# Kernel tuning notes

Hardware: AMD Instinct MI355X
Metric: run time of the kernel (lower is better)

Reference implementation:

```python
import jax, jax.numpy as jnp
import numpy as np

E, H, D = 512, 8, 64          # embed_dim, num_heads, head_dim
MAX_SUM = 128                  # max_summary (embedding table has MAX_SUM+1 rows, row 0 = padding)
SCALE = D ** -0.5


def _linear(x, w, b):
    y = jnp.einsum('...i,oi->...o', x, w)
    return y if b is None else y + b


def setup_inputs() -> dict:
    key = jax.random.key(0)
    ks = jax.random.split(key, 16)
    R, B, S = 2048, 2, 128

    def xav(k, shape, gain=1.0):
        fan_in, fan_out = shape[1], shape[0]
        a = gain * np.sqrt(6.0 / (fan_in + fan_out))
        return jax.random.uniform(k, shape, jnp.float32, -a, a)

    g = 1.0 / np.sqrt(2.0)
    embed_table = jax.random.normal(ks[0], (MAX_SUM + 1, E), jnp.float32) * 0.02
    embed_table = embed_table.at[0].set(0.0)  # padding_idx=0
    return {
        'reg_x': jax.random.normal(ks[1], (R, B, E), jnp.float32),
        'sum_token_ids': jax.random.randint(ks[2], (B, S), 0, MAX_SUM),
        'sum_len': S,
        'reg_len': R,
        'embed_table': embed_table,
        'wq1': xav(ks[3], (E, E), g), 'bq1': jnp.zeros((E,), jnp.float32),
        'wq2': xav(ks[4], (E, E), g), 'bq2': jnp.zeros((E,), jnp.float32),
        'wk': xav(ks[5], (E, E), g),  'bk': jnp.zeros((E,), jnp.float32),
        'wv': xav(ks[6], (E, E), g),  'bv': jnp.zeros((E,), jnp.float32),
        'wo': xav(ks[7], (E, E)),     'bo': jnp.zeros((E,), jnp.float32),
        'sum_gate_w': xav(ks[8], (E, E)),
        'reg_gate_w': xav(ks[9], (E, E)),
        'gate_bias': jax.random.normal(ks[10], (E,), jnp.float32),
    }


def reference(reg_x, sum_token_ids, sum_len, reg_len, embed_table,
              wq1, bq1, wq2, bq2, wk, bk, wv, bv, wo, bo,
              sum_gate_w, reg_gate_w, gate_bias):
    R, B, _ = reg_x.shape
    S = sum_token_ids.shape[1]

    # regular keys/values (shared across all stages)
    reg_k = _linear(reg_x, wk, bk).reshape(R, B, H, D)
    reg_v = _linear(reg_x, wv, bv).reshape(R, B, H, D)

    # ---- stage 1: summary queries (learned summary embeddings) attend to regular tokens
    sum_q = embed_table[sum_token_ids.T].reshape(S, B, H, D)  # [S,B,H,D]
    scores_sr = jnp.einsum('sbhd,rbhd->bhsr', sum_q * SCALE, reg_k)
    w_sr = jax.nn.softmax(scores_sr, axis=-1)
    sum_x2 = jnp.einsum('bhsr,rbhd->sbhd', w_sr, reg_v)       # summary K=V for stage 2

    # ---- stage 2: regular queries attend to summary tokens
    reg_q1 = _linear(reg_x, wq1, bq1).reshape(R, B, H, D)
    scores_rs = jnp.einsum('rbhd,sbhd->bhrs', reg_q1 * SCALE, sum_x2)
    w_rs = jax.nn.softmax(scores_rs, axis=-1)
    sum_output = jnp.einsum('bhrs,sbhd->rbhd', w_rs, sum_x2).reshape(R, B, E)

    # ---- stage 3: regular self-attention
    reg_q2 = _linear(reg_x, wq2, bq2).reshape(R, B, H, D)
    scores_rr = jnp.einsum('qbhd,kbhd->bhqk', reg_q2 * SCALE, reg_k)
    w_rr = jax.nn.softmax(scores_rr, axis=-1)
    reg_output = jnp.einsum('bhqk,kbhd->qbhd', w_rr, reg_v).reshape(R, B, E)

    # ---- gated fusion of summary path and regular path
    gate = jax.nn.sigmoid(_linear(sum_output, sum_gate_w, None)
                          + _linear(reg_output, reg_gate_w, None) + gate_bias)
    attn_output = gate * sum_output + (1.0 - gate) * reg_output
    return _linear(attn_output, wo, bo)
```

## Files before the change

### kernel.cpp

```cpp
#include <hip/hip_runtime.h>
#include <cstdint>
#include <cstddef>

constexpr int R_ = 2048;
constexpr int B_ = 2;
constexpr int S_ = 128;
constexpr int E_ = 512;
constexpr int H_ = 8;
constexpr int D_ = 64;
constexpr int N_ = R_ * B_;
constexpr float SCALE_ = 0.125f;
constexpr float LOG2E_ = 1.44269504088896340736f;
constexpr float SLOG2E_ = SCALE_ * LOG2E_;

typedef short bf8_t __attribute__((ext_vector_type(8)));
typedef float f32x4 __attribute__((ext_vector_type(4)));
typedef float f32x16 __attribute__((ext_vector_type(16)));
typedef unsigned u32x4 __attribute__((ext_vector_type(4)));

#define MFMA16(a, b, c) __builtin_amdgcn_mfma_f32_16x16x32_bf16((a), (b), (c), 0, 0, 0)
#define MFMA32(a, b, c) __builtin_amdgcn_mfma_f32_32x32x16_bf16((a), (b), (c), 0, 0, 0)

__device__ __forceinline__ unsigned short f2bf(float f) {
  unsigned u = __builtin_bit_cast(unsigned, f);
  unsigned r = u + 0x7FFFu + ((u >> 16) & 1u);
  return (unsigned short)(r >> 16);
}
__device__ __forceinline__ float bf2f(unsigned short h) {
  unsigned u = ((unsigned)h) << 16;
  return __builtin_bit_cast(float, u);
}
__device__ __forceinline__ int kvperm(int kv) {
  return (kv & ~15) | (kv & 3) | ((kv & 4) << 1) | ((kv & 8) >> 1);
}

struct WSplitJob { const float* src; unsigned short* dst; };
struct WSplit7 { WSplitJob j[7]; };

__global__ __launch_bounds__(256)
void fused_split_kernel(const float* __restrict__ reg_x, unsigned short* __restrict__ Apair,
                        WSplit7 P, const float* __restrict__ table,
                        const int* __restrict__ ids,
                        unsigned short* __restrict__ sqhi, unsigned short* __restrict__ sqlo)
{
  const int bx = blockIdx.x;
  const int tid = threadIdx.x;
  if (bx < 8192) {
    const int idx = bx * 256 + tid;
    const int r = idx >> 9, c = idx & 511;
    const float v = reg_x[idx];
    const unsigned short hi = f2bf(v);
    unsigned short* d = Apair + ((size_t)r << 10) + c;
    d[0] = hi; d[512] = f2bf(v - bf2f(hi));
  } else if (bx < 15360) {
    const int bj = bx - 8192;
    const WSplitJob jb = P.j[bj >> 10];
    const int idx = (bj & 1023) * 256 + tid;
    const int r = idx >> 9, c = idx & 511;
    const float v = jb.src[idx];
    const unsigned short hi = f2bf(v);
    const unsigned short lo = f2bf(v - bf2f(hi));
    unsigned short* d = jb.dst + (size_t)r * 1536 + c;
    d[0] = hi; d[512] = hi; d[1024] = lo;
  } else {
    const int idx = (bx - 15360) * 256 + tid;
    const int d = idx & 63;
    const int s = (idx >> 6) & 127;
    const int h = (idx >> 13) & 7;
    const int b = idx >> 16;
    const float v = table[(size_t)ids[b * S_ + s] * E_ + h * 64 + d] * SLOG2E_;
    const unsigned short hi = f2bf(v);
    sqhi[idx] = hi;
    sqlo[idx] = f2bf(v - bf2f(hi));
  }
}

struct GemmOut {
  const unsigned short* W;
  const float* bias;
  float scale;
  float* Cf;
  unsigned short* hi;
  unsigned short* lo;
  int mode;
};
struct GemmOuts4 { GemmOut o[4]; };

__global__ __launch_bounds__(256, 4)
void gemm_split_kernel(const unsigned short* __restrict__ A, GemmOuts4 P)
{
  const GemmOut g = P.o[blockIdx.z];
  __shared__ unsigned short As[128][48];
  __shared__ unsigned short Ws[64][48];

  const int tid = threadIdx.x;
  const int w = tid >> 6;
  const int l = tid & 63;
  const int lr = l & 15;
  const int lg = l >> 4;
  const int n0 = blockIdx.x * 128;
  const int o0 = blockIdx.y * 64;

  f32x4 acc[2][4];
#pragma unroll
  for (int m = 0; m < 2; ++m)
#pragma unroll
    for (int n = 0; n < 4; ++n) acc[m][n] = (f32x4){0.f, 0.f, 0.f, 0.f};

  const int ar = tid >> 1;
  const int ac = (tid & 1) * 16;
  const int wr = tid >> 2;
  const int wc = (tid & 3) * 8;

  bf8_t ra0 = *(const bf8_t*)(A + (size_t)(n0 + ar) * 1024 + ac);
  bf8_t ra1 = *(const bf8_t*)(A + (size_t)(n0 + ar) * 1024 + ac + 8);
  bf8_t rw0 = *(const bf8_t*)(g.W + (size_t)(o0 + wr) * 1536 + wc);

  for (int k0 = 0; k0 < 1536; k0 += 32) {
    __syncthreads();
    *(bf8_t*)&As[ar][ac] = ra0;
    *(bf8_t*)&As[ar][ac + 8] = ra1;
    *(bf8_t*)&Ws[wr][wc] = rw0;
    __syncthreads();
    if (k0 + 32 < 1536) {
      const int ak = (k0 + 32) & 1023;
      ra0 = *(const bf8_t*)(A + (size_t)(n0 + ar) * 1024 + ak + ac);
      ra1 = *(const bf8_t*)(A + (size_t)(n0 + ar) * 1024 + ak + ac + 8);
      rw0 = *(const bf8_t*)(g.W + (size_t)(o0 + wr) * 1536 + k0 + 32 + wc);
    }

    bf8_t bvs[4];
#pragma unroll
    for (int n = 0; n < 4; ++n)
      bvs[n] = *(const bf8_t*)&Ws[n * 16 + lr][lg * 8];
#pragma unroll
    for (int m = 0; m < 2; ++m) {
      bf8_t av = *(const bf8_t*)&As[w * 32 + m * 16 + lr][lg * 8];
#pragma unroll
      for (int n = 0; n < 4; ++n)
        acc[m][n] = MFMA16(av, bvs[n], acc[m][n]);
    }
  }

#pragma unroll
  for (int m = 0; m < 2; ++m)
#pragma unroll
    for (int n = 0; n < 4; ++n)
#pragma unroll
      for (int r = 0; r < 4; ++r) {
        const int row = n0 + w * 32 + m * 16 + lg * 4 + r;
        const int col = o0 + n * 16 + lr;
        float v = acc[m][n][r];
        if (g.bias) v += g.bias[col];
        v *= g.scale;
        if (g.mode == 0) {
          g.Cf[((size_t)row << 9) + col] = v;
        } else {
          const int bb = row & 1, rr = row >> 1;
          const int hh = col >> 6, dd = col & 63;
          size_t id;
          if (g.mode == 1) id = (((size_t)(bb * H_ + hh) * R_) + rr) * 64 + dd;
          else             id = (((size_t)(bb * H_ + hh) * 64) + dd) * R_ + kvperm(rr);
          const unsigned short hv = f2bf(v);
          g.hi[id] = hv;
          g.lo[id] = f2bf(v - bf2f(hv));
        }
      }
}

__global__ __launch_bounds__(256, 4)
void gate_blend_gemm_kernel(const unsigned short* __restrict__ A1,
                            const unsigned short* __restrict__ A2,
                            const unsigned short* __restrict__ W1,
                            const unsigned short* __restrict__ W2,
                            const float* __restrict__ gb,
                            unsigned short* __restrict__ attnP)
{
  __shared__ unsigned short As[128][48];
  __shared__ unsigned short Ws[64][48];

  const int tid = threadIdx.x;
  const int w = tid >> 6;
  const int l = tid & 63;
  const int lr = l & 15;
  const int lg = l >> 4;
  const int n0 = blockIdx.x * 128;
  const int o0 = blockIdx.y * 64;

  f32x4 acc[2][4];
#pragma unroll
  for (int m = 0; m < 2; ++m)
#pragma unroll
    for (int n = 0; n < 4; ++n) acc[m][n] = (f32x4){0.f, 0.f, 0.f, 0.f};

  const int ar = tid >> 1;
  const int ac = (tid & 1) * 16;
  const int wr = tid >> 2;
  const int wc = (tid & 3) * 8;

  auto aP = [&](int kk) {
    const unsigned short* Ax = (kk < 48) ? A1 : A2;
    const int k0 = ((kk < 48) ? kk : kk - 48) * 32;
    return Ax + (size_t)(n0 + ar) * 1024 + (k0 & 1023) + ac;
  };
  auto wP = [&](int kk) {
    const unsigned short* Wx = (kk < 48) ? W1 : W2;
    const int k0 = ((kk < 48) ? kk : kk - 48) * 32;
    return Wx + (size_t)(o0 + wr) * 1536 + k0 + wc;
  };

  bf8_t ra0 = *(const bf8_t*)aP(0);
  bf8_t ra1 = *(const bf8_t*)(aP(0) + 8);
  bf8_t rw0 = *(const bf8_t*)wP(0);

  for (int kk = 0; kk < 96; ++kk) {
    __syncthreads();
    *(bf8_t*)&As[ar][ac] = ra0;
    *(bf8_t*)&As[ar][ac + 8] = ra1;
    *(bf8_t*)&Ws[wr][wc] = rw0;
    __syncthreads();
    if (kk + 1 < 96) {
      ra0 = *(const bf8_t*)aP(kk + 1);
      ra1 = *(const bf8_t*)(aP(kk + 1) + 8);
      rw0 = *(const bf8_t*)wP(kk + 1);
    }

    bf8_t bvs[4];
#pragma unroll
    for (int n = 0; n < 4; ++n)
      bvs[n] = *(const bf8_t*)&Ws[n * 16 + lr][lg * 8];
#pragma unroll
    for (int m = 0; m < 2; ++m) {
      bf8_t av = *(const bf8_t*)&As[w * 32 + m * 16 + lr][lg * 8];
#pragma unroll
      for (int n = 0; n < 4; ++n)
        acc[m][n] = MFMA16(av, bvs[n], acc[m][n]);
    }
  }

#pragma unroll
  for (int m = 0; m < 2; ++m)
#pragma unroll
    for (int n = 0; n < 4; ++n)
#pragma unroll
      for (int r = 0; r < 4; ++r) {
        const int row = n0 + w * 32 + m * 16 + lg * 4 + r;
        const int col = o0 + n * 16 + lr;
        const float t = acc[m][n][r] + gb[col];
        const float gt = 1.0f / (1.0f + __expf(-t));
        const size_t base = (size_t)row << 10;
        const float so = bf2f(A1[base + col]) + bf2f(A1[base + 512 + col]);
        const float ro = bf2f(A2[base + col]) + bf2f(A2[base + 512 + col]);
        const float a = gt * so + (1.0f - gt) * ro;
        const unsigned short hv = f2bf(a);
        attnP[base + col] = hv;
        attnP[base + 512 + col] = f2bf(a - bf2f(hv));
      }
}

struct FArgs {
  const unsigned short *Qhi, *Qlo, *Khi, *Klo, *VtHi, *VtLo;
  int q_len, kv_len, chunk, zsplit, out_mode;
  float *accA, *accB, *mlP;
  unsigned short* OutP;
};

__device__ __forceinline__
void flash_body(const FArgs& A, const int bh, const int q0blk, const int c)
{
  __shared__ unsigned short KsH[64][72];
  __shared__ unsigned short KsL[64][72];
  __shared__ unsigned short VsH[64][72];
  __shared__ unsigned short VsL[64][72];

  const int tid = threadIdx.x;
  const int w = tid >> 6;
  const int l = tid & 63;
  const int lq = l & 31;
  const int hi = l >> 5;
  const int q0 = q0blk * 128;
  const int kvbeg = c * A.chunk;
  const int kvend = kvbeg + A.chunk;
  const int qrow = q0 + w * 32 + lq;

  bf8_t qh[4], ql[4];
  {
    const size_t qbase = ((size_t)bh * A.q_len + qrow) * 64;
#pragma unroll
    for (int kd = 0; kd < 4; ++kd) {
      qh[kd] = *(const bf8_t*)(A.Qhi + qbase + kd * 16 + hi * 8);
      ql[kd] = *(const bf8_t*)(A.Qlo + qbase + kd * 16 + hi * 8);
    }
  }

  f32x16 acc0 = {0,0,0,0,0,0,0,0,0,0,0,0,0,0,0,0};
  f32x16 acc1 = {0,0,0,0,0,0,0,0,0,0,0,0,0,0,0,0};
  float mrow = -INFINITY;
  float lrow = 0.0f;

  const int sr = tid >> 2;
  const int sc = (tid & 3) * 16;

  bf8_t rkh[2], rkl[2], rvh[2], rvl[2];
  {
    const size_t kb = ((size_t)bh * A.kv_len + kvbeg + sr) * 64 + sc;
    rkh[0] = *(const bf8_t*)(A.Khi + kb);  rkh[1] = *(const bf8_t*)(A.Khi + kb + 8);
    rkl[0] = *(const bf8_t*)(A.Klo + kb);  rkl[1] = *(const bf8_t*)(A.Klo + kb + 8);
    const size_t vb = ((size_t)bh * 64 + sr) * A.kv_len + kvbeg + sc;
    rvh[0] = *(const bf8_t*)(A.VtHi + vb); rvh[1] = *(const bf8_t*)(A.VtHi + vb + 8);
    rvl[0] = *(const bf8_t*)(A.VtLo + vb); rvl[1] = *(const bf8_t*)(A.VtLo + vb + 8);
  }

  for (int kv0 = kvbeg; kv0 < kvend; kv0 += 64) {
    __syncthreads();
    *(bf8_t*)&KsH[sr][sc] = rkh[0];  *(bf8_t*)&KsH[sr][sc + 8] = rkh[1];
    *(bf8_t*)&KsL[sr][sc] = rkl[0];  *(bf8_t*)&KsL[sr][sc + 8] = rkl[1];
    *(bf8_t*)&VsH[sr][sc] = rvh[0];  *(bf8_t*)&VsH[sr][sc + 8] = rvh[1];
    *(bf8_t*)&VsL[sr][sc] = rvl[0];  *(bf8_t*)&VsL[sr][sc + 8] = rvl[1];
    __syncthreads();
    if (kv0 + 64 < kvend) {
      const size_t kb = ((size_t)bh * A.kv_len + kv0 + 64 + sr) * 64 + sc;
      rkh[0] = *(const bf8_t*)(A.Khi + kb);  rkh[1] = *(const bf8_t*)(A.Khi + kb + 8);
      rkl[0] = *(const bf8_t*)(A.Klo + kb);  rkl[1] = *(const bf8_t*)(A.Klo + kb + 8);
      const size_t vb = ((size_t)bh * 64 + sr) * A.kv_len + kv0 + 64 + sc;
      rvh[0] = *(const bf8_t*)(A.VtHi + vb); rvh[1] = *(const bf8_t*)(A.VtHi + vb + 8);
      rvl[0] = *(const bf8_t*)(A.VtLo + vb); rvl[1] = *(const bf8_t*)(A.VtLo + vb + 8);
    }

    f32x16 s0 = {0,0,0,0,0,0,0,0,0,0,0,0,0,0,0,0};
    f32x16 s1 = {0,0,0,0,0,0,0,0,0,0,0,0,0,0,0,0};
    __builtin_amdgcn_s_setprio(1);
#pragma unroll
    for (int kd = 0; kd < 4; ++kd) {
      const bf8_t kfh0 = *(const bf8_t*)&KsH[lq][kd * 16 + hi * 8];
      const bf8_t kfl0 = *(const bf8_t*)&KsL[lq][kd * 16 + hi * 8];
      s0 = MFMA32(kfh0, qh[kd], s0);
      s0 = MFMA32(kfh0, ql[kd], s0);
      s0 = MFMA32(kfl0, qh[kd], s0);
      const bf8_t kfh1 = *(const bf8_t*)&KsH[32 + lq][kd * 16 + hi * 8];
      const bf8_t kfl1 = *(const bf8_t*)&KsL[32 + lq][kd * 16 + hi * 8];
      s1 = MFMA32(kfh1, qh[kd], s1);
      s1 = MFMA32(kfh1, ql[kd], s1);
      s1 = MFMA32(kfl1, qh[kd], s1);
    }
    __builtin_amdgcn_s_setprio(0);

    float mx = fmaxf(s0[0], s1[0]);
#pragma unroll
    for (int r = 1; r < 16; ++r) mx = fmaxf(mx, fmaxf(s0[r], s1[r]));
    mx = fmaxf(mx, __shfl_xor(mx, 32));
    if (mx > mrow + 8.0f) {
      const float f = exp2f(mrow - mx);
      mrow = mx;
      lrow *= f;
#pragma unroll
      for (int r = 0; r < 16; ++r) { acc0[r] *= f; acc1[r] *= f; }
    }
    float ts = 0.f;
#pragma unroll
    for (int r = 0; r < 16; ++r) { s0[r] = exp2f(s0[r] - mrow); ts += s0[r]; }
#pragma unroll
    for (int r = 0; r < 16; ++r) { s1[r] = exp2f(s1[r] - mrow); ts += s1[r]; }
    ts += __shfl_xor(ts, 32);
    lrow += ts;

    bf8_t pah[4], pal[4];
    const unsigned sel = 0x07060302u;
#pragma unroll
    for (int n = 0; n < 2; ++n)
#pragma unroll
      for (int ks = 0; ks < 2; ++ks) {
        u32x4 hp, lp;
#pragma unroll
        for (int p2 = 0; p2 < 4; ++p2) {
          const float a = n ? s1[ks * 8 + p2 * 2]     : s0[ks * 8 + p2 * 2];
          const float b = n ? s1[ks * 8 + p2 * 2 + 1] : s0[ks * 8 + p2 * 2 + 1];
          const unsigned ua = __builtin_bit_cast(unsigned, a);
          const unsigned ub = __builtin_bit_cast(unsigned, b);
          hp[p2] = __builtin_amdgcn_perm(ub, ua, sel);
          const float la = a - __builtin_bit_cast(float, ua & 0xFFFF0000u);
          const float lb = b - __builtin_bit_cast(float, ub & 0xFFFF0000u);
          lp[p2] = __builtin_amdgcn_perm(__builtin_bit_cast(unsigned, lb),
                                         __builtin_bit_cast(unsigned, la), sel);
        }
        pah[n * 2 + ks] = __builtin_bit_cast(bf8_t, hp);
        pal[n * 2 + ks] = __builtin_bit_cast(bf8_t, lp);
      }

    __builtin_amdgcn_s_setprio(1);
#pragma unroll
    for (int n = 0; n < 2; ++n)
#pragma unroll
      for (int ks = 0; ks < 2; ++ks) {
        const int vcol = n * 32 + ks * 16 + hi * 8;
        const bf8_t ph = pah[n * 2 + ks];
        const bf8_t pl = pal[n * 2 + ks];
        {
          const bf8_t vfh = *(const bf8_t*)&VsH[lq][vcol];
          const bf8_t vfl = *(const bf8_t*)&VsL[lq][vcol];
          acc0 = MFMA32(vfh, ph, acc0);
          acc0 = MFMA32(vfh, pl, acc0);
          acc0 = MFMA32(vfl, ph, acc0);
        }
        {
          const bf8_t vfh = *(const bf8_t*)&VsH[32 + lq][vcol];
          const bf8_t vfl = *(const bf8_t*)&VsL[32 + lq][vcol];
          acc1 = MFMA32(vfh, ph, acc1);
          acc1 = MFMA32(vfh, pl, acc1);
          acc1 = MFMA32(vfl, ph, acc1);
        }
      }
    __builtin_amdgcn_s_setprio(0);
  }

  if (A.out_mode == 0) {
    const size_t cstride = (size_t)16 * A.q_len * 64;
    float* accbase = (c < A.zsplit) ? A.accA + (size_t)c * cstride
                                    : A.accB + (size_t)(c - A.zsplit) * cstride;
    float* rowp = accbase + ((size_t)bh * A.q_len + qrow) * 64;
#pragma unroll
    for (int rg = 0; rg < 4; ++rg) {
      *(float4*)(rowp + rg * 8 + hi * 4) =
          make_float4(acc0[rg * 4 + 0], acc0[rg * 4 + 1], acc0[rg * 4 + 2], acc0[rg * 4 + 3]);
      *(float4*)(rowp + 32 + rg * 8 + hi * 4) =
          make_float4(acc1[rg * 4 + 0], acc1[rg * 4 + 1], acc1[rg * 4 + 2], acc1[rg * 4 + 3]);
    }
    if (l < 32) {
      const int q = q0 + w * 32 + l;
      *(float2*)&A.mlP[((size_t)(c * 16 + bh) * A.q_len + q) * 2] = make_float2(mrow, lrow);
    }
  } else {
    const float inv = 1.0f / lrow;
    const int b = bh >> 3, h = bh & 7;
    const size_t base = ((size_t)qrow * B_ + b) << 10;
#pragma unroll
    for (int hd = 0; hd < 2; ++hd)
#pragma unroll
      for (int rg = 0; rg < 4; ++rg) {
        const int col = h * 64 + hd * 32 + rg * 8 + hi * 4;
        ushort4 hv4, lv4;
#pragma unroll
        for (int i = 0; i < 4; ++i) {
          const float v = (hd ? acc1[rg * 4 + i] : acc0[rg * 4 + i]) * inv;
          const unsigned short hv = f2bf(v);
          ((unsigned short*)&hv4)[i] = hv;
          ((unsigned short*)&lv4)[i] = f2bf(v - bf2f(hv));
        }
        *(ushort4*)&A.OutP[base + col] = hv4;
        *(ushort4*)&A.OutP[base + 512 + col] = lv4;
      }
  }
}

__global__ __launch_bounds__(256, 2)
void flash_s1_kernel(FArgs a)
{
  flash_body(a, blockIdx.x, blockIdx.y, blockIdx.z);
}

__global__ __launch_bounds__(256, 2)
void flash_s23_kernel(FArgs a3, FArgs a2)
{
  const int bid = blockIdx.x;
  if (bid < 512) flash_body(a3, bid & 15, (bid >> 4) & 15, bid >> 8);
  else           flash_body(a2, bid & 15, ((bid - 512) >> 4) & 15, 0);
}

__global__ __launch_bounds__(256)
void merge_x2_kernel(const float* __restrict__ acc, const float* __restrict__ ml,
                     unsigned short* __restrict__ X2hi, unsigned short* __restrict__ X2lo,
                     unsigned short* __restrict__ X2Thi, unsigned short* __restrict__ X2Tlo)
{
  const int idx = blockIdx.x * 256 + threadIdx.x;
  const int d = idx & 63;
  const int q = (idx >> 6) & 127;
  const int bh = idx >> 13;
  float M = -INFINITY;
#pragma unroll
  for (int c = 0; c < 16; ++c)
    M = fmaxf(M, ml[((size_t)(c * 16 + bh) * 128 + q) * 2]);
  float ls = 0.f, o = 0.f;
#pragma unroll
  for (int c = 0; c < 16; ++c) {
    const size_t mi = ((size_t)(c * 16 + bh) * 128 + q) * 2;
    const float wgt = exp2f(ml[mi] - M);
    ls += wgt * ml[mi + 1];
    o += wgt * acc[(size_t)c * 131072 + ((size_t)bh * 128 + q) * 64 + d];
  }
  const float v = o / ls;
  const unsigned short hv = f2bf(v);
  const unsigned short lv = f2bf(v - bf2f(hv));
  X2hi[((size_t)bh * 128 + q) * 64 + d] = hv;
  X2lo[((size_t)bh * 128 + q) * 64 + d] = lv;
  const int qp = kvperm(q);
  X2Thi[((size_t)bh * 64 + d) * 128 + qp] = hv;
  X2Tlo[((size_t)bh * 64 + d) * 128 + qp] = lv;
}

__global__ __launch_bounds__(256)
void merge_rows_kernel(const float* __restrict__ accA, const float* __restrict__ accB,
                       const float* __restrict__ ml, unsigned short* __restrict__ OutP)
{
  const int idx = blockIdx.x * 256 + threadIdx.x;
  const int d = idx & 63;
  const int q = (idx >> 6) & 2047;
  const int bh = idx >> 17;
  const size_t mi0 = ((size_t)bh * 2048 + q) * 2;
  const size_t mi1 = ((size_t)(16 + bh) * 2048 + q) * 2;
  const float m0 = ml[mi0], m1 = ml[mi1];
  const float M = fmaxf(m0, m1);
  const float w0 = exp2f(m0 - M), w1 = exp2f(m1 - M);
  const float ls = w0 * ml[mi0 + 1] + w1 * ml[mi1 + 1];
  const size_t aoff = ((size_t)bh * 2048 + q) * 64 + d;
  const float v = (w0 * accA[aoff] + w1 * accB[aoff]) / ls;
  const int b = bh >> 3, h = bh & 7;
  const size_t nrow = (size_t)q * B_ + b;
  const int col = h * 64 + d;
  const unsigned short hv = f2bf(v);
  OutP[nrow * 1024 + col] = hv;
  OutP[nrow * 1024 + 512 + col] = f2bf(v - bf2f(hv));
}

extern "C" void kernel_launch(void* const* d_in, const int* in_sizes, int n_in,
                              void* d_out, int out_size, void* d_ws, size_t ws_size,
                              hipStream_t stream)
{
  const float* reg_x = (const float*)d_in[0];
  const int*   ids   = (const int*)d_in[1];
  const float* table = (const float*)d_in[4];
  const float* wq1 = (const float*)d_in[5];  const float* bq1 = (const float*)d_in[6];
  const float* wq2 = (const float*)d_in[7];  const float* bq2 = (const float*)d_in[8];
  const float* wk  = (const float*)d_in[9];  const float* bk  = (const float*)d_in[10];
  const float* wv  = (const float*)d_in[11]; const float* bv  = (const float*)d_in[12];
  const float* wo  = (const float*)d_in[13]; const float* bo  = (const float*)d_in[14];
  const float* sgw = (const float*)d_in[15];
  const float* rgw = (const float*)d_in[16];
  const float* gb  = (const float*)d_in[17];
  float* out = (float*)d_out;
  char* W = (char*)d_ws;

  const size_t WSLOT  = 1572864;
  const size_t oApair = 0;
  const size_t oW     = 8388608;
  const size_t oKhi   = oW + 7 * WSLOT;
  const size_t oKlo   = oKhi + 4194304;
  const size_t oVtHi  = oKlo + 4194304;
  const size_t oVtLo  = oVtHi + 4194304;
  const size_t oQ1hi  = oVtLo + 4194304;
  const size_t oQ1lo  = oQ1hi + 4194304;
  const size_t oQ2hi  = oQ1lo + 4194304;
  const size_t oQ2lo  = oQ2hi + 4194304;
  const size_t oAcc1  = oQ2lo + 4194304;
  const size_t oSQhi  = oAcc1 + 8388608;
  const size_t oSQlo  = oSQhi + 262144;
  const size_t oX2hi  = oSQlo + 262144;
  const size_t oX2lo  = oX2hi + 262144;
  const size_t oX2Thi = oX2lo + 262144;
  const size_t oX2Tlo = oX2Thi + 262144;
  const size_t oMl    = oX2Tlo + 262144;

  auto U16 = [&](size_t off) { return (unsigned short*)(W + off); };
  auto F32 = [&](size_t off) { return (float*)(W + off); };
  unsigned short* Apair  = U16(oApair);
  unsigned short* Wk3    = U16(oW + 0 * WSLOT);
  unsigned short* Wv3    = U16(oW + 1 * WSLOT);
  unsigned short* Wq13   = U16(oW + 2 * WSLOT);
  unsigned short* Wq23   = U16(oW + 3 * WSLOT);
  unsigned short* Wsg3   = U16(oW + 4 * WSLOT);
  unsigned short* Wrg3   = U16(oW + 5 * WSLOT);
  unsigned short* Wo3    = U16(oW + 6 * WSLOT);
  float*          accS   = F32(oApair);
  float*          accB3  = F32(oAcc1);
  float*          mlP    = F32(oMl);
  unsigned short* sout_p = U16(oQ1hi);
  unsigned short* rout_p = U16(oQ2hi);
  unsigned short* attn_p = U16(oKhi);

  const dim3 blk(256);

  WSplit7 ws7;
  ws7.j[0] = WSplitJob{wk,  Wk3};
  ws7.j[1] = WSplitJob{wv,  Wv3};
  ws7.j[2] = WSplitJob{wq1, Wq13};
  ws7.j[3] = WSplitJob{wq2, Wq23};
  ws7.j[4] = WSplitJob{sgw, Wsg3};
  ws7.j[5] = WSplitJob{rgw, Wrg3};
  ws7.j[6] = WSplitJob{wo,  Wo3};
  fused_split_kernel<<<15872, blk, 0, stream>>>(reg_x, Apair, ws7, table, ids,
                                                U16(oSQhi), U16(oSQlo));

  GemmOuts4 proj;
  proj.o[0].W = Wk3;  proj.o[0].bias = bk;  proj.o[0].scale = 1.0f;    proj.o[0].Cf = nullptr;
  proj.o[0].hi = U16(oKhi);  proj.o[0].lo = U16(oKlo);  proj.o[0].mode = 1;
  proj.o[1].W = Wv3;  proj.o[1].bias = bv;  proj.o[1].scale = 1.0f;    proj.o[1].Cf = nullptr;
  proj.o[1].hi = U16(oVtHi); proj.o[1].lo = U16(oVtLo); proj.o[1].mode = 2;
  proj.o[2].W = Wq13; proj.o[2].bias = bq1; proj.o[2].scale = SLOG2E_; proj.o[2].Cf = nullptr;
  proj.o[2].hi = U16(oQ1hi); proj.o[2].lo = U16(oQ1lo); proj.o[2].mode = 1;
  proj.o[3].W = Wq23; proj.o[3].bias = bq2; proj.o[3].scale = SLOG2E_; proj.o[3].Cf = nullptr;
  proj.o[3].hi = U16(oQ2hi); proj.o[3].lo = U16(oQ2lo); proj.o[3].mode = 1;
  gemm_split_kernel<<<dim3(32, 8, 4), blk, 0, stream>>>(Apair, proj);

  FArgs a1;
  a1.Qhi = U16(oSQhi); a1.Qlo = U16(oSQlo);
  a1.Khi = U16(oKhi);  a1.Klo = U16(oKlo);
  a1.VtHi = U16(oVtHi); a1.VtLo = U16(oVtLo);
  a1.q_len = S_; a1.kv_len = R_; a1.chunk = 128; a1.zsplit = 16; a1.out_mode = 0;
  a1.accA = accS; a1.accB = accS; a1.mlP = mlP; a1.OutP = nullptr;
  flash_s1_kernel<<<dim3(16, 1, 16), blk, 0, stream>>>(a1);
  merge_x2_kernel<<<512, blk, 0, stream>>>(accS, mlP,
      U16(oX2hi), U16(oX2lo), U16(oX2Thi), U16(oX2Tlo));

  FArgs a3;
  a3.Qhi = U16(oQ2hi); a3.Qlo = U16(oQ2lo);
  a3.Khi = U16(oKhi);  a3.Klo = U16(oKlo);
  a3.VtHi = U16(oVtHi); a3.VtLo = U16(oVtLo);
  a3.q_len = R_; a3.kv_len = R_; a3.chunk = 1024; a3.zsplit = 1; a3.out_mode = 0;
  a3.accA = accS; a3.accB = accB3; a3.mlP = mlP; a3.OutP = nullptr;
  FArgs a2;
  a2.Qhi = U16(oQ1hi); a2.Qlo = U16(oQ1lo);
  a2.Khi = U16(oX2hi); a2.Klo = U16(oX2lo);
  a2.VtHi = U16(oX2Thi); a2.VtLo = U16(oX2Tlo);
  a2.q_len = R_; a2.kv_len = S_; a2.chunk = 128; a2.zsplit = 1; a2.out_mode = 1;
  a2.accA = nullptr; a2.accB = nullptr; a2.mlP = mlP; a2.OutP = sout_p;
  flash_s23_kernel<<<768, blk, 0, stream>>>(a3, a2);

  merge_rows_kernel<<<8192, blk, 0, stream>>>(accS, accB3, mlP, rout_p);

  gate_blend_gemm_kernel<<<dim3(32, 8), blk, 0, stream>>>(
      sout_p, rout_p, Wsg3, Wrg3, gb, attn_p);

  GemmOuts4 gf;
  gf.o[0].W = Wo3; gf.o[0].bias = bo; gf.o[0].scale = 1.0f; gf.o[0].Cf = out;
  gf.o[0].hi = nullptr; gf.o[0].lo = nullptr; gf.o[0].mode = 0;
  gf.o[1] = gf.o[0]; gf.o[2] = gf.o[0]; gf.o[3] = gf.o[0];
  gemm_split_kernel<<<dim3(32, 8, 1), blk, 0, stream>>>(attn_p, gf);
}
```

Measured before the change: 222.4 us.

## Replace projection GEMM with 128x128-tile double-buffered kernel using direct global-to-LDS loads

Swaps the QKV projection GEMM for a new kernel that uses 128x128 output tiles instead of 128x64. It double-buffers shared memory, filling it with global_load_lds direct copies so the next K-slice is fetched while MFMAs run. It also raises wave priority around the MFMA block. The goal is more operand reuse per tile and hidden load latency, at the cost of fewer blocks (512), lower occupancy (3 per CU) and more register pressure from the 16 accumulators.

```diff
diff --git a/kernel.cpp b/kernel.cpp
--- a/kernel.cpp
+++ b/kernel.cpp
@@ -32,6 +32,11 @@
 }
 __device__ __forceinline__ int kvperm(int kv) {
   return (kv & ~15) | (kv & 3) | ((kv & 4) << 1) | ((kv & 8) >> 1);
+}
+__device__ __forceinline__ void gload16(const unsigned short* g, unsigned short* l) {
+  __builtin_amdgcn_global_load_lds(
+      (const __attribute__((address_space(1))) unsigned*)g,
+      (__attribute__((address_space(3))) unsigned*)l, 16, 0, 0);
 }
 
 struct WSplitJob { const float* src; unsigned short* dst; };
@@ -168,6 +173,102 @@
       }
 }
 
+struct GOut {
+  const unsigned short* W;
+  const float* bias;
+  float scale;
+  unsigned short* hi;
+  unsigned short* lo;
+  int mode;
+};
+struct GOuts4 { GOut o[4]; };
+
+__global__ __launch_bounds__(256, 3)
+void gemm128_kernel(const unsigned short* __restrict__ A, GOuts4 P)
+{
+  const GOut g = P.o[blockIdx.z];
+  __shared__ unsigned short As[2][4096];
+  __shared__ unsigned short Ws[2][4096];
+
+  const int tid = threadIdx.x;
+  const int w = tid >> 6;
+  const int l = tid & 63;
+  const int lr = l & 15;
+  const int lg = l >> 4;
+  const int wr = (w >> 1) * 64;
+  const int wc = (w & 1) * 64;
+  const int n0 = blockIdx.x * 128;
+  const int o0 = blockIdx.y * 128;
+
+  const int srow = w * 32 + (l >> 2);
+  const int scol = (l & 3) * 8;
+  const unsigned short* A0 = A + (size_t)(n0 + srow) * 1024 + scol;
+  const unsigned short* A1 = A0 + (size_t)16 * 1024;
+  const unsigned short* W0 = g.W + (size_t)(o0 + srow) * 1536 + scol;
+  const unsigned short* W1 = W0 + (size_t)16 * 1536;
+
+  f32x4 acc[4][4];
+#pragma unroll
+  for (int m = 0; m < 4; ++m)
+#pragma unroll
+    for (int n = 0; n < 4; ++n) acc[m][n] = (f32x4){0.f, 0.f, 0.f, 0.f};
+
+  gload16(A0, &As[0][w * 1024]);
+  gload16(A1, &As[0][w * 1024 + 512]);
+  gload16(W0, &Ws[0][w * 1024]);
+  gload16(W1, &Ws[0][w * 1024 + 512]);
+  __syncthreads();
+
+  int buf = 0;
+  for (int t = 0; t < 48; ++t) {
+    if (t + 1 < 48) {
+      const int ak = ((t + 1) * 32) & 1023;
+      const int wk = (t + 1) * 32;
+      gload16(A0 + ak, &As[buf ^ 1][w * 1024]);
+      gload16(A1 + ak, &As[buf ^ 1][w * 1024 + 512]);
+      gload16(W0 + wk, &Ws[buf ^ 1][w * 1024]);
+      gload16(W1 + wk, &Ws[buf ^ 1][w * 1024 + 512]);
+    }
+    bf8_t av[4], bv[4];
+#pragma unroll
+    for (int m = 0; m < 4; ++m)
+      av[m] = *(const bf8_t*)&As[buf][(wr + m * 16 + lr) * 32 + lg * 8];
+#pragma unroll
+    for (int n = 0; n < 4; ++n)
+      bv[n] = *(const bf8_t*)&Ws[buf][(wc + n * 16 + lr) * 32 + lg * 8];
+    __builtin_amdgcn_s_setprio(1);
+#pragma unroll
+    for (int m = 0; m < 4; ++m)
+#pragma unroll
+      for (int n = 0; n < 4; ++n)
+        acc[m][n] = MFMA16(av[m], bv[n], acc[m][n]);
+    __builtin_amdgcn_s_setprio(0);
+    __syncthreads();
+    buf ^= 1;
+  }
+
+#pragma unroll
+  for (int m = 0; m < 4; ++m)
+#pragma unroll
+    for (int n = 0; n < 4; ++n)
+#pragma unroll
+      for (int r = 0; r < 4; ++r) {
+        const int row = n0 + wr + m * 16 + lg * 4 + r;
+        const int col = o0 + wc + n * 16 + lr;
+        float v = acc[m][n][r];
+        if (g.bias) v += g.bias[col];
+        v *= g.scale;
+        const int bb = row & 1, rr = row >> 1;
+        const int hh = col >> 6, dd = col & 63;
+        size_t id;
+        if (g.mode == 1) id = (((size_t)(bb * H_ + hh) * R_) + rr) * 64 + dd;
+        else             id = (((size_t)(bb * H_ + hh) * 64) + dd) * R_ + kvperm(rr);
+        const unsigned short hv = f2bf(v);
+        g.hi[id] = hv;
+        g.lo[id] = f2bf(v - bf2f(hv));
+      }
+}
+
 __global__ __launch_bounds__(256, 4)
 void gate_blend_gemm_kernel(const unsigned short* __restrict__ A1,
                             const unsigned short* __restrict__ A2,
@@ -589,16 +690,12 @@
   fused_split_kernel<<<15872, blk, 0, stream>>>(reg_x, Apair, ws7, table, ids,
                                                 U16(oSQhi), U16(oSQlo));
 
-  GemmOuts4 proj;
-  proj.o[0].W = Wk3;  proj.o[0].bias = bk;  proj.o[0].scale = 1.0f;    proj.o[0].Cf = nullptr;
-  proj.o[0].hi = U16(oKhi);  proj.o[0].lo = U16(oKlo);  proj.o[0].mode = 1;
-  proj.o[1].W = Wv3;  proj.o[1].bias = bv;  proj.o[1].scale = 1.0f;    proj.o[1].Cf = nullptr;
-  proj.o[1].hi = U16(oVtHi); proj.o[1].lo = U16(oVtLo); proj.o[1].mode = 2;
-  proj.o[2].W = Wq13; proj.o[2].bias = bq1; proj.o[2].scale = SLOG2E_; proj.o[2].Cf = nullptr;
-  proj.o[2].hi = U16(oQ1hi); proj.o[2].lo = U16(oQ1lo); proj.o[2].mode = 1;
-  proj.o[3].W = Wq23; proj.o[3].bias = bq2; proj.o[3].scale = SLOG2E_; proj.o[3].Cf = nullptr;
-  proj.o[3].hi = U16(oQ2hi); proj.o[3].lo = U16(oQ2lo); proj.o[3].mode = 1;
-  gemm_split_kernel<<<dim3(32, 8, 4), blk, 0, stream>>>(Apair, proj);
+  GOuts4 proj;
+  proj.o[0] = GOut{Wk3,  bk,  1.0f,    U16(oKhi),  U16(oKlo),  1};
+  proj.o[1] = GOut{Wv3,  bv,  1.0f,    U16(oVtHi), U16(oVtLo), 2};
+  proj.o[2] = GOut{Wq13, bq1, SLOG2E_, U16(oQ1hi), U16(oQ1lo), 1};
+  proj.o[3] = GOut{Wq23, bq2, SLOG2E_, U16(oQ2hi), U16(oQ2lo), 1};
+  gemm128_kernel<<<dim3(32, 4, 4), blk, 0, stream>>>(Apair, proj);
 
   FArgs a1;
   a1.Qhi = U16(oSQhi); a1.Qlo = U16(oSQlo);
```

After: 222.4 us. No clear change (+0.0%).
